# Optimization experiments

Hardware: AMD Instinct MI355X
Metric: run time of the kernel (lower is better)

## Reference

```python
import jax, jax.numpy as jnp
import numpy as np
import math

B, N, H = 2, 2048, 256
NUM_HEADS, HEAD_DIM = 8, 32
WIN = 32            # window_size
WIN_LEN = 2 * WIN + 1


def setup_inputs() -> dict:
    key = jax.random.key(0)
    ks = jax.random.split(key, 12)
    s = 0.02
    return {
        "x": jax.random.normal(ks[0], (B, N, 4, H), dtype=jnp.float32),
        "Wq": jax.random.normal(ks[1], (H, H), dtype=jnp.float32) * s,
        "bq": jnp.zeros((H,), jnp.float32),
        "Wk": jax.random.normal(ks[2], (H, H), dtype=jnp.float32) * s,
        "bk": jnp.zeros((H,), jnp.float32),
        "Wv": jax.random.normal(ks[3], (H, H), dtype=jnp.float32) * s,
        "bv": jnp.zeros((H,), jnp.float32),
        "Wo": jax.random.normal(ks[4], (H, 3 * H), dtype=jnp.float32) * s,
        "bo": jnp.zeros((3 * H,), jnp.float32),
        "Wvec": jax.random.normal(ks[5], (H, 2 * H), dtype=jnp.float32) * s,
        "alpha_dot": jnp.float32(1.0),
        "alpha_norm": jnp.float32(1.0),
        "Wg": jax.random.normal(ks[6], (2 * H, H), dtype=jnp.float32) * s,
        "bg": jnp.zeros((H,), jnp.float32),
    }


def reference(x, Wq, bq, Wk, bk, Wv, bv, Wo, bo, Wvec, alpha_dot, alpha_norm, Wg, bg):
    h, d = NUM_HEADS, HEAD_DIM
    scale = 1.0 / math.sqrt(d)

    x_scalar = x[:, :, 0]          # (B,N,H)
    vec = x[:, :, 1:4]             # (B,N,3,H)

    q = (x_scalar @ Wq + bq).reshape(B, N, h, d).transpose(0, 2, 1, 3)  # (B,h,N,d)
    k = (x_scalar @ Wk + bk).reshape(B, N, h, d).transpose(0, 2, 1, 3)
    v = (x_scalar @ Wv + bv).reshape(B, N, h, d).transpose(0, 2, 1, 3)

    vec_proj = vec @ Wvec                                # (B,N,3,2H)
    vec1, vec2 = vec_proj[..., :H], vec_proj[..., H:]
    vec_dot = (vec1 * vec2).sum(axis=-2)                 # (B,N,H)
    vec_norm = jnp.linalg.norm(vec, axis=2)              # (B,N,H)

    # (B,N,3,h,d) -> (B,h,N,3*d)
    vec_flat = vec.reshape(B, N, 3, h, d).transpose(0, 3, 1, 2, 4).reshape(B, h, N, 3 * d)

    # sliding-window attention via padded gather (matches torch unfold semantics)
    BH = B * h
    q_l = q.reshape(BH, N, d)
    k_l = k.reshape(BH, N, d)
    v_l = v.reshape(BH, N, d)
    vec_l = vec_flat.reshape(BH, N, 3 * d)

    pad = ((0, 0), (WIN, WIN), (0, 0))
    k_p = jnp.pad(k_l, pad)
    v_p = jnp.pad(v_l, pad)
    vec_p = jnp.pad(vec_l, pad)

    idx = jnp.arange(N)[:, None] + jnp.arange(WIN_LEN)[None, :]  # (N,WIN_LEN)
    k_win = k_p[:, idx]        # (BH,N,WIN_LEN,d)
    v_win = v_p[:, idx]
    vec_win = vec_p[:, idx]    # (BH,N,WIN_LEN,3d)

    attn_scores = jnp.einsum('bid,biwd->biw', q_l, k_win) * scale
    attn_weights = jax.nn.softmax(attn_scores, axis=-1)  # (BH,N,WIN_LEN)

    x_agg = jnp.einsum('biw,biwd->bid', attn_weights, v_win).reshape(B, h, N, d)
    vec_aggr = jnp.einsum('biw,biwd->bid', attn_weights, vec_win).reshape(B, h, N, 3 * d)

    x_out = x_agg.transpose(0, 2, 1, 3).reshape(B, N, H)
    vec_aggr = vec_aggr.reshape(B, h, N, 3, d).transpose(0, 2, 3, 1, 4).reshape(B, N, 3, H)

    invariants = jnp.concatenate([alpha_dot * vec_dot, alpha_norm * vec_norm], axis=-1)
    gate = jax.nn.sigmoid(invariants @ Wg + bg)[:, :, None, :]   # (B,N,1,H)
    vec_combined = gate * vec_aggr + vec                          # gated add mixing

    o = x_out @ Wo + bo
    o1, o2, o3 = o[..., :H], o[..., H:2 * H], o[..., 2 * H:]
    x_updated = vec_dot * o1 + vec_norm * o2 + o3

    x_final = jnp.concatenate([x_updated[:, :, None], vec_combined], axis=2)  # (B,N,4,H)
    return x_final, attn_weights
```

## Files before the change

kernel.cpp:

```cpp
#include <hip/hip_runtime.h>
#include <hip/hip_bf16.h>
#include <math.h>

#define Bc 2
#define Nn 2048
#define Hh 256
#define NH 8
#define Dd 32
#define WIN 32
#define WL 65
#define BN (Bc * Nn)

typedef __attribute__((ext_vector_type(8))) short bf16x8;
typedef __attribute__((ext_vector_type(4))) float f32x4;

__device__ inline short f2bf(float f) {
    union { float f; unsigned u; } v; v.f = f;
    unsigned r = v.u + 0x7fffu + ((v.u >> 16) & 1u);
    return (short)(r >> 16);
}

__device__ inline bf16x8 cvt8(float4 a, float4 b) {
    union { __hip_bfloat162 h[4]; bf16x8 v; } u;
    u.h[0] = __float22bfloat162_rn(make_float2(a.x, a.y));
    u.h[1] = __float22bfloat162_rn(make_float2(a.z, a.w));
    u.h[2] = __float22bfloat162_rn(make_float2(b.x, b.y));
    u.h[3] = __float22bfloat162_rn(make_float2(b.z, b.w));
    return u.v;
}

__global__ __launch_bounds__(256) void castw_kernel(
    const float* __restrict__ Wq, const float* __restrict__ Wk, const float* __restrict__ Wv,
    const float* __restrict__ Wvec, const float* __restrict__ Wg, const float* __restrict__ Wo,
    short* __restrict__ WqkvT, short* __restrict__ WvecT,
    short* __restrict__ WgT, short* __restrict__ WoT) {
    __shared__ float Ts[32][33];
    const int t = threadIdx.x;
    const int cc = t & 31, r0 = t >> 5;
    const int id = blockIdx.x;
    const float* W; int ldw; short* WT; int ldwt; int n0s, k0, n0d;
    if (id < 192) {
        const int tn = id >> 3, tk = id & 7, sel = tn >> 3;
        W = sel == 0 ? Wq : (sel == 1 ? Wk : Wv); ldw = 256;
        n0s = (tn & 7) * 32; k0 = tk * 32; WT = WqkvT; ldwt = 256; n0d = tn * 32;
    } else if (id < 320) {
        const int id2 = id - 192, tn = id2 >> 3, tk = id2 & 7;
        W = Wvec; ldw = 512; n0s = tn * 32; k0 = tk * 32; WT = WvecT; ldwt = 256; n0d = n0s;
    } else if (id < 448) {
        const int id3 = id - 320, tn = id3 >> 4, tk = id3 & 15;
        W = Wg; ldw = 256; n0s = tn * 32; k0 = tk * 32; WT = WgT; ldwt = 512; n0d = n0s;
    } else {
        const int id4 = id - 448, tn = id4 >> 3, tk = id4 & 7;
        W = Wo; ldw = 768; n0s = tn * 32; k0 = tk * 32; WT = WoT; ldwt = 256; n0d = n0s;
    }
#pragma unroll
    for (int p = 0; p < 4; ++p) {
        const int rr = r0 + p * 8;
        Ts[rr][cc] = W[(size_t)(k0 + rr) * ldw + n0s + cc];
    }
    __syncthreads();
#pragma unroll
    for (int p = 0; p < 4; ++p) {
        const int rr = r0 + p * 8;
        WT[(size_t)(n0d + rr) * ldwt + k0 + cc] = f2bf(Ts[cc][rr]);
    }
}

__global__ __launch_bounds__(256) void fused_mid(
    const float* __restrict__ x,
    const short* __restrict__ WqkvT, const short* __restrict__ WvecT,
    const short* __restrict__ WgT,
    const float* __restrict__ bq, const float* __restrict__ bk, const float* __restrict__ bv,
    const float* __restrict__ alpha_dot, const float* __restrict__ alpha_norm,
    const float* __restrict__ bg,
    short* __restrict__ Qb, short* __restrict__ Kb, short* __restrict__ Vb,
    float* __restrict__ vec_dot, float* __restrict__ vec_norm, float* __restrict__ gate) {
    __shared__ __align__(16) short lds[31232];
    const int bid = blockIdx.x;
    const int t = threadIdx.x, lane = t & 63, wid = t >> 6;
    const int quad = lane >> 4, lm = lane & 15;

    if (bid < 384) {
        short* As = lds;
        short* Bs = lds + 2560;
        const int rb = bid & 63, cb = bid >> 6;
        const int row0 = rb * 64, col0 = cb * 128;
        const int wm = wid & 1, wn = wid >> 1;
        const int srow = t >> 2, scg = (t & 3) * 8;
        f32x4 acc[2][4];
#pragma unroll
        for (int mt = 0; mt < 2; ++mt)
#pragma unroll
            for (int nt = 0; nt < 4; ++nt) {
                f32x4 z = {0.f, 0.f, 0.f, 0.f};
                acc[mt][nt] = z;
            }
        float4 pa0 = *(const float4*)&x[(size_t)(row0 + srow) * 1024 + scg];
        float4 pa1 = *(const float4*)&x[(size_t)(row0 + srow) * 1024 + scg + 4];
        bf16x8 pb[2];
#pragma unroll
        for (int p = 0; p < 2; ++p) {
            const int idx = t + p * 256;
            pb[p] = *(const bf16x8*)&WqkvT[(size_t)(col0 + (idx >> 2)) * 256 + (idx & 3) * 8];
        }
        for (int k0 = 0; k0 < 256; k0 += 32) {
            *(bf16x8*)&As[srow * 40 + scg] = cvt8(pa0, pa1);
#pragma unroll
            for (int p = 0; p < 2; ++p) {
                const int idx = t + p * 256;
                *(bf16x8*)&Bs[(idx >> 2) * 40 + (idx & 3) * 8] = pb[p];
            }
            __syncthreads();
            if (k0 + 32 < 256) {
                pa0 = *(const float4*)&x[(size_t)(row0 + srow) * 1024 + k0 + 32 + scg];
                pa1 = *(const float4*)&x[(size_t)(row0 + srow) * 1024 + k0 + 32 + scg + 4];
#pragma unroll
                for (int p = 0; p < 2; ++p) {
                    const int idx = t + p * 256;
                    pb[p] = *(const bf16x8*)&WqkvT[(size_t)(col0 + (idx >> 2)) * 256 + k0 + 32 + (idx & 3) * 8];
                }
            }
            bf16x8 af[2], bfr[4];
#pragma unroll
            for (int mt = 0; mt < 2; ++mt)
                af[mt] = *(bf16x8*)&As[(wm * 32 + mt * 16 + lm) * 40 + quad * 8];
#pragma unroll
            for (int nt = 0; nt < 4; ++nt)
                bfr[nt] = *(bf16x8*)&Bs[(wn * 64 + nt * 16 + lm) * 40 + quad * 8];
#pragma unroll
            for (int mt = 0; mt < 2; ++mt)
#pragma unroll
                for (int nt = 0; nt < 4; ++nt)
                    acc[mt][nt] = __builtin_amdgcn_mfma_f32_16x16x32_bf16(
                        af[mt], bfr[nt], acc[mt][nt], 0, 0, 0);
            __syncthreads();
        }
        const int chunk = col0 >> 8;
        short* dst = chunk == 0 ? Qb : (chunk == 1 ? Kb : Vb);
        const float* bias = chunk == 0 ? bq : (chunk == 1 ? bk : bv);
#pragma unroll
        for (int mt = 0; mt < 2; ++mt)
#pragma unroll
            for (int nt = 0; nt < 4; ++nt) {
                const int col = col0 + (wid >> 1) * 64 + nt * 16 + lm;
                const int cm = col & 255;
                const float bb = bias[cm];
#pragma unroll
                for (int r = 0; r < 4; ++r) {
                    const int row = row0 + (wid & 1) * 32 + mt * 16 + quad * 4 + r;
                    dst[(size_t)row * 256 + cm] = f2bf(acc[mt][nt][r] + bb);
                }
            }
        return;
    }

    short* As    = lds;
    short* Bs    = lds + 12672;
    short* inv_s = lds + 22912;
    const int row0 = (bid - 384) * 16;

#pragma unroll
    for (int it = 0; it < 6; ++it) {
        const int idx = t + it * 256;
        const int p = idx >> 9, rem = idx & 511, row = rem >> 5, kg = rem & 31;
        const float* src = &x[(size_t)(row0 + row) * 1024 + (1 + p) * 256 + kg * 8];
        *(bf16x8*)&As[(p * 16 + row) * 264 + kg * 8] =
            cvt8(*(const float4*)src, *(const float4*)(src + 4));
    }
    const float an = alpha_norm[0], ad = alpha_dot[0];
#pragma unroll
    for (int it = 0; it < 4; ++it) {
        const int idx = t + it * 256;
        const int row = idx >> 6, c4 = idx & 63;
        const size_t xb = (size_t)(row0 + row) * 1024 + c4 * 4;
        const float4 v0 = *(const float4*)&x[xb + 256];
        const float4 v1 = *(const float4*)&x[xb + 512];
        const float4 v2 = *(const float4*)&x[xb + 768];
        float4 nr;
        nr.x = sqrtf(v0.x * v0.x + v1.x * v1.x + v2.x * v2.x);
        nr.y = sqrtf(v0.y * v0.y + v1.y * v1.y + v2.y * v2.y);
        nr.z = sqrtf(v0.z * v0.z + v1.z * v1.z + v2.z * v2.z);
        nr.w = sqrtf(v0.w * v0.w + v1.w * v1.w + v2.w * v2.w);
        *(float4*)&vec_norm[(size_t)(row0 + row) * 256 + c4 * 4] = nr;
        short* ip = &inv_s[row * 520 + 256 + c4 * 4];
        ip[0] = f2bf(an * nr.x); ip[1] = f2bf(an * nr.y);
        ip[2] = f2bf(an * nr.z); ip[3] = f2bf(an * nr.w);
    }
    __syncthreads();

    for (int cg = 0; cg < 2; ++cg) {
        f32x4 acc[3][2][2];
#pragma unroll
        for (int p = 0; p < 3; ++p)
#pragma unroll
            for (int h = 0; h < 2; ++h)
#pragma unroll
                for (int nt = 0; nt < 2; ++nt) {
                    f32x4 z = {0.f, 0.f, 0.f, 0.f};
                    acc[p][h][nt] = z;
                }
        bf16x8 pb[4];
#pragma unroll
        for (int q = 0; q < 4; ++q) {
            const int idx = t + q * 256;
            const int h = idx >> 9, rem = idx & 511, col = rem >> 2, kg = rem & 3;
            pb[q] = *(const bf16x8*)&WvecT[(size_t)(h * 256 + cg * 128 + col) * 256 + kg * 8];
        }
        for (int k0 = 0; k0 < 256; k0 += 32) {
#pragma unroll
            for (int q = 0; q < 4; ++q) {
                const int idx = t + q * 256;
                const int h = idx >> 9, rem = idx & 511, col = rem >> 2, kg = rem & 3;
                *(bf16x8*)&Bs[(h * 128 + col) * 40 + kg * 8] = pb[q];
            }
            __syncthreads();
            if (k0 + 32 < 256) {
#pragma unroll
                for (int q = 0; q < 4; ++q) {
                    const int idx = t + q * 256;
                    const int h = idx >> 9, rem = idx & 511, col = rem >> 2, kg = rem & 3;
                    pb[q] = *(const bf16x8*)&WvecT[(size_t)(h * 256 + cg * 128 + col) * 256 + k0 + 32 + kg * 8];
                }
            }
            bf16x8 af[3], bfr[2][2];
#pragma unroll
            for (int p = 0; p < 3; ++p)
                af[p] = *(bf16x8*)&As[(p * 16 + lm) * 264 + k0 + quad * 8];
#pragma unroll
            for (int h = 0; h < 2; ++h)
#pragma unroll
                for (int nt = 0; nt < 2; ++nt)
                    bfr[h][nt] = *(bf16x8*)&Bs[(h * 128 + wid * 32 + nt * 16 + lm) * 40 + quad * 8];
#pragma unroll
            for (int p = 0; p < 3; ++p)
#pragma unroll
                for (int h = 0; h < 2; ++h)
#pragma unroll
                    for (int nt = 0; nt < 2; ++nt)
                        acc[p][h][nt] = __builtin_amdgcn_mfma_f32_16x16x32_bf16(
                            af[p], bfr[h][nt], acc[p][h][nt], 0, 0, 0);
            __syncthreads();
        }
#pragma unroll
        for (int nt = 0; nt < 2; ++nt) {
            const int col = cg * 128 + wid * 32 + nt * 16 + lm;
#pragma unroll
            for (int r = 0; r < 4; ++r) {
                const int row = quad * 4 + r;
                float dot = 0.f;
#pragma unroll
                for (int p = 0; p < 3; ++p)
                    dot = fmaf(acc[p][0][nt][r], acc[p][1][nt][r], dot);
                vec_dot[(size_t)(row0 + row) * 256 + col] = dot;
                inv_s[row * 520 + col] = f2bf(ad * dot);
            }
        }
        __syncthreads();
    }

    f32x4 g[4];
#pragma unroll
    for (int nt = 0; nt < 4; ++nt) {
        f32x4 z = {0.f, 0.f, 0.f, 0.f};
        g[nt] = z;
    }
    bf16x8 pg[4];
#pragma unroll
    for (int q = 0; q < 4; ++q) {
        const int idx = t + q * 256;
        pg[q] = *(const bf16x8*)&WgT[(size_t)(idx >> 2) * 512 + (idx & 3) * 8];
    }
    for (int k0 = 0; k0 < 512; k0 += 32) {
#pragma unroll
        for (int q = 0; q < 4; ++q) {
            const int idx = t + q * 256;
            *(bf16x8*)&Bs[(idx >> 2) * 40 + (idx & 3) * 8] = pg[q];
        }
        __syncthreads();
        if (k0 + 32 < 512) {
#pragma unroll
            for (int q = 0; q < 4; ++q) {
                const int idx = t + q * 256;
                pg[q] = *(const bf16x8*)&WgT[(size_t)(idx >> 2) * 512 + k0 + 32 + (idx & 3) * 8];
            }
        }
        const bf16x8 ai = *(bf16x8*)&inv_s[lm * 520 + k0 + quad * 8];
#pragma unroll
        for (int nt = 0; nt < 4; ++nt) {
            const bf16x8 bgf = *(bf16x8*)&Bs[(wid * 64 + nt * 16 + lm) * 40 + quad * 8];
            g[nt] = __builtin_amdgcn_mfma_f32_16x16x32_bf16(ai, bgf, g[nt], 0, 0, 0);
        }
        __syncthreads();
    }
#pragma unroll
    for (int nt = 0; nt < 4; ++nt) {
        const int col = wid * 64 + nt * 16 + lm;
        const float bb = bg[col];
#pragma unroll
        for (int r = 0; r < 4; ++r) {
            const int row = row0 + quad * 4 + r;
            const float z = g[nt][r] + bb;
            gate[(size_t)row * 256 + col] = 1.f / (1.f + __expf(-z));
        }
    }
}

__global__ __launch_bounds__(256) void attn_fused(
    const short* __restrict__ Qb, const short* __restrict__ Kb,
    const short* __restrict__ Vb,
    const float* __restrict__ gate, const float* __restrict__ x,
    float* __restrict__ attnw, float* __restrict__ out, short* __restrict__ xout_bf) {
    const int bh = blockIdx.x >> 6, tile = blockIdx.x & 63;
    const int b = bh >> 3, hd = bh & 7;
    const int i0 = tile * 32;
    const int t = threadIdx.x, lane = t & 63, wid = t >> 6;
    const int wm = wid & 1, wn = wid >> 1, quad = lane >> 4, lm = lane & 15;

    __shared__ __align__(16) short Qs[32 * 40];
    __shared__ __align__(16) short Ks[96 * 40];
    __shared__ __align__(16) short Pb[32 * 104];
    __shared__ __align__(16) short St[128 * 104];

    for (int idx = t; idx < 32 * 104 / 2; idx += 256) ((int*)Pb)[idx] = 0;
    if (t < 128) {
        const int row = t >> 2, cg = t & 3;
        *(bf16x8*)&Qs[row * 40 + cg * 8] =
            *(const bf16x8*)&Qb[((size_t)(b * Nn + i0 + row)) * 256 + hd * 32 + cg * 8];
    }
#pragma unroll
    for (int kk = 0; kk < 2; ++kk) {
        const int idx = t + kk * 256;
        if (idx < 384) {
            const int row = idx >> 2, cg = idx & 3;
            const int j = i0 - WIN + row;
            bf16x8 kv = {0, 0, 0, 0, 0, 0, 0, 0};
            if (j >= 0 && j < Nn)
                kv = *(const bf16x8*)&Kb[((size_t)(b * Nn + j)) * 256 + hd * 32 + cg * 8];
            *(bf16x8*)&Ks[row * 40 + cg * 8] = kv;
        }
    }
    __syncthreads();

    if (wid < 2) {
        const int il0 = wid * 16;
        const bf16x8 aq = *(bf16x8*)&Qs[(il0 + lm) * 40 + quad * 8];
        f32x4 c[6];
#pragma unroll
        for (int nt = 0; nt < 6; ++nt) {
            const bf16x8 bk = *(bf16x8*)&Ks[(nt * 16 + lm) * 40 + quad * 8];
            f32x4 z = {0.f, 0.f, 0.f, 0.f};
            c[nt] = __builtin_amdgcn_mfma_f32_16x16x32_bf16(aq, bk, z, 0, 0, 0);
        }
        float mx[4] = {-1e30f, -1e30f, -1e30f, -1e30f};
#pragma unroll
        for (int nt = 0; nt < 6; ++nt)
#pragma unroll
            for (int r = 0; r < 4; ++r) {
                const int il = il0 + quad * 4 + r;
                const int w = nt * 16 + lm - il;
                const float v = (w >= 0 && w <= 64)
                    ? c[nt][r] * 0.17677669529663687f : -1e30f;
                c[nt][r] = v;
                mx[r] = fmaxf(mx[r], v);
            }
#pragma unroll
        for (int off = 1; off < 16; off <<= 1)
#pragma unroll
            for (int r = 0; r < 4; ++r) mx[r] = fmaxf(mx[r], __shfl_xor(mx[r], off, 64));
        float sm[4] = {0.f, 0.f, 0.f, 0.f};
#pragma unroll
        for (int nt = 0; nt < 6; ++nt)
#pragma unroll
            for (int r = 0; r < 4; ++r) {
                const int il = il0 + quad * 4 + r;
                const int w = nt * 16 + lm - il;
                const float e = (w >= 0 && w <= 64) ? __expf(c[nt][r] - mx[r]) : 0.f;
                c[nt][r] = e;
                sm[r] += e;
            }
#pragma unroll
        for (int off = 1; off < 16; off <<= 1)
#pragma unroll
            for (int r = 0; r < 4; ++r) sm[r] += __shfl_xor(sm[r], off, 64);
        float inv[4];
#pragma unroll
        for (int r = 0; r < 4; ++r) inv[r] = 1.f / sm[r];
#pragma unroll
        for (int nt = 0; nt < 6; ++nt)
#pragma unroll
            for (int r = 0; r < 4; ++r) {
                const int il = il0 + quad * 4 + r;
                const int jr = nt * 16 + lm;
                const int w = jr - il;
                if (w >= 0 && w <= 64) {
                    const float pw = c[nt][r] * inv[r];
                    attnw[((size_t)bh * Nn + (i0 + il)) * WL + w] = pw;
                    Pb[il * 104 + jr] = f2bf(pw);
                }
            }
    } else {
        const int tt = t - 128;
        const int chunk = tt >> 3, j0 = tt & 7;
#pragma unroll
        for (int it = 0; it < 12; ++it) {
            const int jr = j0 + it * 8;
            const int j = i0 - WIN + jr;
            bf16x8 val = {0, 0, 0, 0, 0, 0, 0, 0};
            if (j >= 0 && j < Nn) {
                if (chunk < 4) {
                    val = *(const bf16x8*)&Vb[((size_t)(b * Nn + j)) * 256 + hd * 32 + chunk * 8];
                } else {
                    const int vc = (chunk - 4) >> 2, d0 = ((chunk - 4) & 3) * 8;
                    const float* src = &x[((size_t)(b * Nn + j)) * 1024 + (1 + vc) * 256 + hd * 32 + d0];
                    val = cvt8(*(const float4*)src, *(const float4*)(src + 4));
                }
            }
#pragma unroll
            for (int u = 0; u < 8; ++u) St[(chunk * 8 + u) * 104 + jr] = val[u];
        }
    }
    __syncthreads();

    f32x4 acc[4];
#pragma unroll
    for (int nt = 0; nt < 4; ++nt) {
        f32x4 z = {0.f, 0.f, 0.f, 0.f};
        acc[nt] = z;
    }
#pragma unroll
    for (int ks = 0; ks < 3; ++ks) {
        const bf16x8 ap = *(bf16x8*)&Pb[(wm * 16 + lm) * 104 + ks * 32 + quad * 8];
#pragma unroll
        for (int nt = 0; nt < 4; ++nt) {
            const bf16x8 bs = *(bf16x8*)&St[(wn * 64 + nt * 16 + lm) * 104 + ks * 32 + quad * 8];
            acc[nt] = __builtin_amdgcn_mfma_f32_16x16x32_bf16(ap, bs, acc[nt], 0, 0, 0);
        }
    }
#pragma unroll
    for (int nt = 0; nt < 4; ++nt) {
        const int dim = wn * 64 + nt * 16 + lm;
#pragma unroll
        for (int r = 0; r < 4; ++r) {
            const int i = wm * 16 + quad * 4 + r;
            const size_t bn = (size_t)(b * Nn + i0 + i);
            if (dim < 32) {
                xout_bf[bn * 256 + hd * 32 + dim] = f2bf(acc[nt][r]);
            } else {
                const int dm = dim - 32, c = dm >> 5, dd = dm & 31;
                const int ch = hd * 32 + dd;
                const float g = gate[bn * 256 + ch];
                const size_t off = bn * 1024 + (1 + c) * 256 + ch;
                out[off] = fmaf(g, acc[nt][r], x[off]);
            }
        }
    }
}

__global__ __launch_bounds__(256) void gemm_outf(
    const short* __restrict__ A, const short* __restrict__ BT,
    const float* __restrict__ bo,
    const float* __restrict__ vec_dot, const float* __restrict__ vec_norm,
    float* __restrict__ out) {
    __shared__ short As[64 * 40];
    __shared__ short Bs[3][64 * 40];
    const int row0 = blockIdx.x * 64, ch0 = blockIdx.y * 64;
    const int t = threadIdx.x, lane = t & 63, wid = t >> 6;
    const int wm = wid & 1, wn = wid >> 1, quad = lane >> 4, lm = lane & 15;
    const int srow = t >> 2, scg = (t & 3) * 8;
    f32x4 acc[3][2][2];
#pragma unroll
    for (int p = 0; p < 3; ++p)
#pragma unroll
        for (int mt = 0; mt < 2; ++mt)
#pragma unroll
            for (int nt = 0; nt < 2; ++nt) {
                f32x4 z = {0.f, 0.f, 0.f, 0.f};
                acc[p][mt][nt] = z;
            }
    bf16x8 pa, pb[3];
    pa = *(const bf16x8*)&A[(size_t)(row0 + srow) * 256 + scg];
#pragma unroll
    for (int p = 0; p < 3; ++p)
        pb[p] = *(const bf16x8*)&BT[(size_t)(p * 256 + ch0 + srow) * 256 + scg];
    for (int k0 = 0; k0 < 256; k0 += 32) {
        *(bf16x8*)&As[srow * 40 + scg] = pa;
#pragma unroll
        for (int p = 0; p < 3; ++p)
            *(bf16x8*)&Bs[p][srow * 40 + scg] = pb[p];
        __syncthreads();
        if (k0 + 32 < 256) {
            pa = *(const bf16x8*)&A[(size_t)(row0 + srow) * 256 + k0 + 32 + scg];
#pragma unroll
            for (int p = 0; p < 3; ++p)
                pb[p] = *(const bf16x8*)&BT[(size_t)(p * 256 + ch0 + srow) * 256 + k0 + 32 + scg];
        }
        bf16x8 af[2], bfr[3][2];
#pragma unroll
        for (int mt = 0; mt < 2; ++mt)
            af[mt] = *(bf16x8*)&As[(wm * 32 + mt * 16 + lm) * 40 + quad * 8];
#pragma unroll
        for (int p = 0; p < 3; ++p)
#pragma unroll
            for (int nt = 0; nt < 2; ++nt)
                bfr[p][nt] = *(bf16x8*)&Bs[p][(wn * 32 + nt * 16 + lm) * 40 + quad * 8];
#pragma unroll
        for (int p = 0; p < 3; ++p)
#pragma unroll
            for (int mt = 0; mt < 2; ++mt)
#pragma unroll
                for (int nt = 0; nt < 2; ++nt)
                    acc[p][mt][nt] = __builtin_amdgcn_mfma_f32_16x16x32_bf16(
                        af[mt], bfr[p][nt], acc[p][mt][nt], 0, 0, 0);
        __syncthreads();
    }
#pragma unroll
    for (int mt = 0; mt < 2; ++mt)
#pragma unroll
        for (int nt = 0; nt < 2; ++nt) {
            const int col = ch0 + wn * 32 + nt * 16 + lm;
            const float b1 = bo[col], b2 = bo[256 + col], b3 = bo[512 + col];
#pragma unroll
            for (int r = 0; r < 4; ++r) {
                const int row = row0 + wm * 32 + mt * 16 + quad * 4 + r;
                const float o1 = acc[0][mt][nt][r] + b1;
                const float o2 = acc[1][mt][nt][r] + b2;
                const float o3 = acc[2][mt][nt][r] + b3;
                const float vd = vec_dot[(size_t)row * 256 + col];
                const float vn = vec_norm[(size_t)row * 256 + col];
                out[(size_t)row * 1024 + col] = vd * o1 + vn * o2 + o3;
            }
        }
}

extern "C" void kernel_launch(void* const* d_in, const int* in_sizes, int n_in,
                              void* d_out, int out_size, void* d_ws, size_t ws_size,
                              hipStream_t stream) {
    const float* x  = (const float*)d_in[0];
    const float* Wq = (const float*)d_in[1];
    const float* bq = (const float*)d_in[2];
    const float* Wk = (const float*)d_in[3];
    const float* bk = (const float*)d_in[4];
    const float* Wv = (const float*)d_in[5];
    const float* bv = (const float*)d_in[6];
    const float* Wo = (const float*)d_in[7];
    const float* bo = (const float*)d_in[8];
    const float* Wvec = (const float*)d_in[9];
    const float* alpha_dot  = (const float*)d_in[10];
    const float* alpha_norm = (const float*)d_in[11];
    const float* Wg = (const float*)d_in[12];
    const float* bg = (const float*)d_in[13];

    float* ws = (float*)d_ws;
    float* vec_dot  = ws;
    float* vec_norm = ws + 1048576;
    float* gate     = ws + 2097152;
    short* sb = (short*)(ws + 3145728);
    short* xout_bf = sb;
    short* Q_bf    = sb + 1048576;
    short* K_bf    = sb + 2097152;
    short* V_bf    = sb + 3145728;
    short* WqkvT   = sb + 4194304;
    short* WvecT   = sb + 4390912;
    short* WgT     = sb + 4521984;
    short* WoT     = sb + 4653056;

    float* out = (float*)d_out;
    float* attnw = out + (size_t)Bc * Nn * 4 * Hh;

    castw_kernel<<<640, 256, 0, stream>>>(Wq, Wk, Wv, Wvec, Wg, Wo,
                                          WqkvT, WvecT, WgT, WoT);
    fused_mid<<<640, 256, 0, stream>>>(x, WqkvT, WvecT, WgT, bq, bk, bv,
                                       alpha_dot, alpha_norm, bg,
                                       Q_bf, K_bf, V_bf, vec_dot, vec_norm, gate);
    attn_fused<<<1024, 256, 0, stream>>>(Q_bf, K_bf, V_bf, gate, x,
                                         attnw, out, xout_bf);
    gemm_outf<<<dim3(64, 4), 256, 0, stream>>>(xout_bf, WoT, bo, vec_dot, vec_norm, out);
}
```

Before: 154.8 us.

## Redistribute vec-norm, vec-dot, gate GEMM across kernels for better parallelism

Moves the vector-norm computation into the weight-cast prep kernel and retiles the vec_dot GEMM in the middle kernel into 64x32 output tiles, giving 512 blocks instead of 256 blocks of 16 rows. The gate GEMM now runs as its own block range alongside attention in a combined kernel. Attention writes vec_aggr to a workspace buffer, and the gated residual add moves into the output GEMM kernel. This is meant to raise occupancy and parallelism in the mid stage, at the cost of extra global round trips for inv_bf and vec_aggr (about 12 MB more traffic).

```diff
diff --git a/kernel.cpp b/kernel.cpp
--- a/kernel.cpp
+++ b/kernel.cpp
@@ -12,6 +12,7 @@
 #define BN (Bc * Nn)
 
 typedef __attribute__((ext_vector_type(8))) short bf16x8;
+typedef __attribute__((ext_vector_type(4))) short s16x4;
 typedef __attribute__((ext_vector_type(4))) float f32x4;
 
 __device__ inline short f2bf(float f) {
@@ -29,13 +30,35 @@
     return u.v;
 }
 
-__global__ __launch_bounds__(256) void castw_kernel(
+__global__ __launch_bounds__(256) void prep_kernel(
+    const float* __restrict__ x, const float* __restrict__ alpha_norm,
     const float* __restrict__ Wq, const float* __restrict__ Wk, const float* __restrict__ Wv,
     const float* __restrict__ Wvec, const float* __restrict__ Wg, const float* __restrict__ Wo,
+    float* __restrict__ vec_norm, short* __restrict__ inv_bf,
     short* __restrict__ WqkvT, short* __restrict__ WvecT,
     short* __restrict__ WgT, short* __restrict__ WoT) {
     __shared__ float Ts[32][33];
     const int t = threadIdx.x;
+    if (blockIdx.x >= 640) {
+        const int gid = (blockIdx.x - 640) * 256 + t;
+        const int bn = gid >> 6, c4 = gid & 63;
+        const size_t base = (size_t)bn * 1024 + c4 * 4;
+        const float4 v0 = *(const float4*)&x[base + 256];
+        const float4 v1 = *(const float4*)&x[base + 512];
+        const float4 v2 = *(const float4*)&x[base + 768];
+        float4 nr;
+        nr.x = sqrtf(v0.x * v0.x + v1.x * v1.x + v2.x * v2.x);
+        nr.y = sqrtf(v0.y * v0.y + v1.y * v1.y + v2.y * v2.y);
+        nr.z = sqrtf(v0.z * v0.z + v1.z * v1.z + v2.z * v2.z);
+        nr.w = sqrtf(v0.w * v0.w + v1.w * v1.w + v2.w * v2.w);
+        *(float4*)&vec_norm[(size_t)bn * 256 + c4 * 4] = nr;
+        const float an = alpha_norm[0];
+        s16x4 iv;
+        iv[0] = f2bf(an * nr.x); iv[1] = f2bf(an * nr.y);
+        iv[2] = f2bf(an * nr.z); iv[3] = f2bf(an * nr.w);
+        *(s16x4*)&inv_bf[(size_t)bn * 512 + 256 + c4 * 4] = iv;
+        return;
+    }
     const int cc = t & 31, r0 = t >> 5;
     const int id = blockIdx.x;
     const float* W; int ldw; short* WT; int ldwt; int n0s, k0, n0d;
@@ -66,27 +89,23 @@
     }
 }
 
-__global__ __launch_bounds__(256) void fused_mid(
+__global__ __launch_bounds__(256) void mid_kernel(
     const float* __restrict__ x,
     const short* __restrict__ WqkvT, const short* __restrict__ WvecT,
-    const short* __restrict__ WgT,
     const float* __restrict__ bq, const float* __restrict__ bk, const float* __restrict__ bv,
-    const float* __restrict__ alpha_dot, const float* __restrict__ alpha_norm,
-    const float* __restrict__ bg,
+    const float* __restrict__ alpha_dot,
     short* __restrict__ Qb, short* __restrict__ Kb, short* __restrict__ Vb,
-    float* __restrict__ vec_dot, float* __restrict__ vec_norm, float* __restrict__ gate) {
-    __shared__ __align__(16) short lds[31232];
+    float* __restrict__ vec_dot, short* __restrict__ inv_bf) {
+    __shared__ __align__(16) short lds[10240];
     const int bid = blockIdx.x;
     const int t = threadIdx.x, lane = t & 63, wid = t >> 6;
-    const int quad = lane >> 4, lm = lane & 15;
+    const int wm = wid & 1, wn = wid >> 1, quad = lane >> 4, lm = lane & 15;
+    const int srow = t >> 2, scg = (t & 3) * 8;
 
     if (bid < 384) {
         short* As = lds;
         short* Bs = lds + 2560;
-        const int rb = bid & 63, cb = bid >> 6;
-        const int row0 = rb * 64, col0 = cb * 128;
-        const int wm = wid & 1, wn = wid >> 1;
-        const int srow = t >> 2, scg = (t & 3) * 8;
+        const int row0 = (bid & 63) * 64, col0 = (bid >> 6) * 128;
         f32x4 acc[2][4];
 #pragma unroll
         for (int mt = 0; mt < 2; ++mt)
@@ -142,184 +161,163 @@
         for (int mt = 0; mt < 2; ++mt)
 #pragma unroll
             for (int nt = 0; nt < 4; ++nt) {
-                const int col = col0 + (wid >> 1) * 64 + nt * 16 + lm;
-                const int cm = col & 255;
+                const int cm = (col0 + wn * 64 + nt * 16 + lm) & 255;
                 const float bb = bias[cm];
 #pragma unroll
                 for (int r = 0; r < 4; ++r) {
-                    const int row = row0 + (wid & 1) * 32 + mt * 16 + quad * 4 + r;
+                    const int row = row0 + wm * 32 + mt * 16 + quad * 4 + r;
                     dst[(size_t)row * 256 + cm] = f2bf(acc[mt][nt][r] + bb);
                 }
             }
         return;
     }
 
-    short* As    = lds;
-    short* Bs    = lds + 12672;
-    short* inv_s = lds + 22912;
-    const int row0 = (bid - 384) * 16;
-
-#pragma unroll
-    for (int it = 0; it < 6; ++it) {
-        const int idx = t + it * 256;
-        const int p = idx >> 9, rem = idx & 511, row = rem >> 5, kg = rem & 31;
-        const float* src = &x[(size_t)(row0 + row) * 1024 + (1 + p) * 256 + kg * 8];
-        *(bf16x8*)&As[(p * 16 + row) * 264 + kg * 8] =
-            cvt8(*(const float4*)src, *(const float4*)(src + 4));
-    }
-    const float an = alpha_norm[0], ad = alpha_dot[0];
-#pragma unroll
-    for (int it = 0; it < 4; ++it) {
-        const int idx = t + it * 256;
-        const int row = idx >> 6, c4 = idx & 63;
-        const size_t xb = (size_t)(row0 + row) * 1024 + c4 * 4;
-        const float4 v0 = *(const float4*)&x[xb + 256];
-        const float4 v1 = *(const float4*)&x[xb + 512];
-        const float4 v2 = *(const float4*)&x[xb + 768];
-        float4 nr;
-        nr.x = sqrtf(v0.x * v0.x + v1.x * v1.x + v2.x * v2.x);
-        nr.y = sqrtf(v0.y * v0.y + v1.y * v1.y + v2.y * v2.y);
-        nr.z = sqrtf(v0.z * v0.z + v1.z * v1.z + v2.z * v2.z);
-        nr.w = sqrtf(v0.w * v0.w + v1.w * v1.w + v2.w * v2.w);
-        *(float4*)&vec_norm[(size_t)(row0 + row) * 256 + c4 * 4] = nr;
-        short* ip = &inv_s[row * 520 + 256 + c4 * 4];
-        ip[0] = f2bf(an * nr.x); ip[1] = f2bf(an * nr.y);
-        ip[2] = f2bf(an * nr.z); ip[3] = f2bf(an * nr.w);
-    }
-    __syncthreads();
-
-    for (int cg = 0; cg < 2; ++cg) {
-        f32x4 acc[3][2][2];
+    short* As = lds;
+    short* Bs = lds + 7680;
+    const int vb = bid - 384;
+    const int row0 = (vb >> 3) * 64, ch0 = (vb & 7) * 32;
+    const int bh_ = t >> 7, bc = (t >> 2) & 31, bcg = (t & 3) * 8;
+    f32x4 acc[3][2][2];
+#pragma unroll
+    for (int p = 0; p < 3; ++p)
+#pragma unroll
+        for (int h = 0; h < 2; ++h)
+#pragma unroll
+            for (int mt = 0; mt < 2; ++mt) {
+                f32x4 z = {0.f, 0.f, 0.f, 0.f};
+                acc[p][h][mt] = z;
+            }
+    float4 pa0[3], pa1[3];
+#pragma unroll
+    for (int p = 0; p < 3; ++p) {
+        pa0[p] = *(const float4*)&x[(size_t)(row0 + srow) * 1024 + (1 + p) * 256 + scg];
+        pa1[p] = *(const float4*)&x[(size_t)(row0 + srow) * 1024 + (1 + p) * 256 + scg + 4];
+    }
+    bf16x8 pb = *(const bf16x8*)&WvecT[(size_t)(bh_ * 256 + ch0 + bc) * 256 + bcg];
+    for (int k0 = 0; k0 < 256; k0 += 32) {
 #pragma unroll
         for (int p = 0; p < 3; ++p)
+            *(bf16x8*)&As[p * 2560 + srow * 40 + scg] = cvt8(pa0[p], pa1[p]);
+        *(bf16x8*)&Bs[bh_ * 1280 + bc * 40 + bcg] = pb;
+        __syncthreads();
+        if (k0 + 32 < 256) {
+#pragma unroll
+            for (int p = 0; p < 3; ++p) {
+                pa0[p] = *(const float4*)&x[(size_t)(row0 + srow) * 1024 + (1 + p) * 256 + k0 + 32 + scg];
+                pa1[p] = *(const float4*)&x[(size_t)(row0 + srow) * 1024 + (1 + p) * 256 + k0 + 32 + scg + 4];
+            }
+            pb = *(const bf16x8*)&WvecT[(size_t)(bh_ * 256 + ch0 + bc) * 256 + k0 + 32 + bcg];
+        }
+        bf16x8 af[3][2], bfr[2];
+#pragma unroll
+        for (int p = 0; p < 3; ++p)
+#pragma unroll
+            for (int mt = 0; mt < 2; ++mt)
+                af[p][mt] = *(bf16x8*)&As[p * 2560 + (wm * 32 + mt * 16 + lm) * 40 + quad * 8];
+#pragma unroll
+        for (int h = 0; h < 2; ++h)
+            bfr[h] = *(bf16x8*)&Bs[h * 1280 + (wn * 16 + lm) * 40 + quad * 8];
+#pragma unroll
+        for (int p = 0; p < 3; ++p)
 #pragma unroll
             for (int h = 0; h < 2; ++h)
 #pragma unroll
-                for (int nt = 0; nt < 2; ++nt) {
-                    f32x4 z = {0.f, 0.f, 0.f, 0.f};
-                    acc[p][h][nt] = z;
+                for (int mt = 0; mt < 2; ++mt)
+                    acc[p][h][mt] = __builtin_amdgcn_mfma_f32_16x16x32_bf16(
+                        af[p][mt], bfr[h], acc[p][h][mt], 0, 0, 0);
+        __syncthreads();
+    }
+    const float ad = alpha_dot[0];
+#pragma unroll
+    for (int mt = 0; mt < 2; ++mt) {
+        const int col = ch0 + wn * 16 + lm;
+#pragma unroll
+        for (int r = 0; r < 4; ++r) {
+            const int row = row0 + wm * 32 + mt * 16 + quad * 4 + r;
+            float dot = 0.f;
+#pragma unroll
+            for (int p = 0; p < 3; ++p)
+                dot = fmaf(acc[p][0][mt][r], acc[p][1][mt][r], dot);
+            vec_dot[(size_t)row * 256 + col] = dot;
+            inv_bf[(size_t)row * 512 + col] = f2bf(ad * dot);
+        }
+    }
+}
+
+__global__ __launch_bounds__(256) void gate_attn_kernel(
+    const short* __restrict__ inv_bf, const short* __restrict__ WgT,
+    const float* __restrict__ bg,
+    const short* __restrict__ Qb, const short* __restrict__ Kb,
+    const short* __restrict__ Vb, const float* __restrict__ x,
+    float* __restrict__ gate, float* __restrict__ attnw,
+    float* __restrict__ vec_aggr, short* __restrict__ xout_bf) {
+    __shared__ __align__(16) short lds[21760];
+    const int bid = blockIdx.x;
+    const int t = threadIdx.x, lane = t & 63, wid = t >> 6;
+    const int wm = wid & 1, wn = wid >> 1, quad = lane >> 4, lm = lane & 15;
+
+    if (bid < 256) {
+        short* As = lds;
+        short* Bs = lds + 2560;
+        const int row0 = (bid & 63) * 64, col0 = (bid >> 6) * 64;
+        const int srow = t >> 2, scg = (t & 3) * 8;
+        f32x4 acc[2][2];
+#pragma unroll
+        for (int mt = 0; mt < 2; ++mt)
+#pragma unroll
+            for (int nt = 0; nt < 2; ++nt) {
+                f32x4 z = {0.f, 0.f, 0.f, 0.f};
+                acc[mt][nt] = z;
+            }
+        bf16x8 pa = *(const bf16x8*)&inv_bf[(size_t)(row0 + srow) * 512 + scg];
+        bf16x8 pb = *(const bf16x8*)&WgT[(size_t)(col0 + srow) * 512 + scg];
+        for (int k0 = 0; k0 < 512; k0 += 32) {
+            *(bf16x8*)&As[srow * 40 + scg] = pa;
+            *(bf16x8*)&Bs[srow * 40 + scg] = pb;
+            __syncthreads();
+            if (k0 + 32 < 512) {
+                pa = *(const bf16x8*)&inv_bf[(size_t)(row0 + srow) * 512 + k0 + 32 + scg];
+                pb = *(const bf16x8*)&WgT[(size_t)(col0 + srow) * 512 + k0 + 32 + scg];
+            }
+            bf16x8 af[2], bfr[2];
+#pragma unroll
+            for (int mt = 0; mt < 2; ++mt)
+                af[mt] = *(bf16x8*)&As[(wm * 32 + mt * 16 + lm) * 40 + quad * 8];
+#pragma unroll
+            for (int nt = 0; nt < 2; ++nt)
+                bfr[nt] = *(bf16x8*)&Bs[(wn * 32 + nt * 16 + lm) * 40 + quad * 8];
+#pragma unroll
+            for (int mt = 0; mt < 2; ++mt)
+#pragma unroll
+                for (int nt = 0; nt < 2; ++nt)
+                    acc[mt][nt] = __builtin_amdgcn_mfma_f32_16x16x32_bf16(
+                        af[mt], bfr[nt], acc[mt][nt], 0, 0, 0);
+            __syncthreads();
+        }
+#pragma unroll
+        for (int mt = 0; mt < 2; ++mt)
+#pragma unroll
+            for (int nt = 0; nt < 2; ++nt) {
+                const int col = col0 + wn * 32 + nt * 16 + lm;
+                const float bb = bg[col];
+#pragma unroll
+                for (int r = 0; r < 4; ++r) {
+                    const int row = row0 + wm * 32 + mt * 16 + quad * 4 + r;
+                    const float z = acc[mt][nt][r] + bb;
+                    gate[(size_t)row * 256 + col] = 1.f / (1.f + __expf(-z));
                 }
-        bf16x8 pb[4];
-#pragma unroll
-        for (int q = 0; q < 4; ++q) {
-            const int idx = t + q * 256;
-            const int h = idx >> 9, rem = idx & 511, col = rem >> 2, kg = rem & 3;
-            pb[q] = *(const bf16x8*)&WvecT[(size_t)(h * 256 + cg * 128 + col) * 256 + kg * 8];
-        }
-        for (int k0 = 0; k0 < 256; k0 += 32) {
-#pragma unroll
-            for (int q = 0; q < 4; ++q) {
-                const int idx = t + q * 256;
-                const int h = idx >> 9, rem = idx & 511, col = rem >> 2, kg = rem & 3;
-                *(bf16x8*)&Bs[(h * 128 + col) * 40 + kg * 8] = pb[q];
-            }
-            __syncthreads();
-            if (k0 + 32 < 256) {
-#pragma unroll
-                for (int q = 0; q < 4; ++q) {
-                    const int idx = t + q * 256;
-                    const int h = idx >> 9, rem = idx & 511, col = rem >> 2, kg = rem & 3;
-                    pb[q] = *(const bf16x8*)&WvecT[(size_t)(h * 256 + cg * 128 + col) * 256 + k0 + 32 + kg * 8];
-                }
-            }
-            bf16x8 af[3], bfr[2][2];
-#pragma unroll
-            for (int p = 0; p < 3; ++p)
-                af[p] = *(bf16x8*)&As[(p * 16 + lm) * 264 + k0 + quad * 8];
-#pragma unroll
-            for (int h = 0; h < 2; ++h)
-#pragma unroll
-                for (int nt = 0; nt < 2; ++nt)
-                    bfr[h][nt] = *(bf16x8*)&Bs[(h * 128 + wid * 32 + nt * 16 + lm) * 40 + quad * 8];
-#pragma unroll
-            for (int p = 0; p < 3; ++p)
-#pragma unroll
-                for (int h = 0; h < 2; ++h)
-#pragma unroll
-                    for (int nt = 0; nt < 2; ++nt)
-                        acc[p][h][nt] = __builtin_amdgcn_mfma_f32_16x16x32_bf16(
-                            af[p], bfr[h][nt], acc[p][h][nt], 0, 0, 0);
-            __syncthreads();
-        }
-#pragma unroll
-        for (int nt = 0; nt < 2; ++nt) {
-            const int col = cg * 128 + wid * 32 + nt * 16 + lm;
-#pragma unroll
-            for (int r = 0; r < 4; ++r) {
-                const int row = quad * 4 + r;
-                float dot = 0.f;
-#pragma unroll
-                for (int p = 0; p < 3; ++p)
-                    dot = fmaf(acc[p][0][nt][r], acc[p][1][nt][r], dot);
-                vec_dot[(size_t)(row0 + row) * 256 + col] = dot;
-                inv_s[row * 520 + col] = f2bf(ad * dot);
-            }
-        }
-        __syncthreads();
-    }
-
-    f32x4 g[4];
-#pragma unroll
-    for (int nt = 0; nt < 4; ++nt) {
-        f32x4 z = {0.f, 0.f, 0.f, 0.f};
-        g[nt] = z;
-    }
-    bf16x8 pg[4];
-#pragma unroll
-    for (int q = 0; q < 4; ++q) {
-        const int idx = t + q * 256;
-        pg[q] = *(const bf16x8*)&WgT[(size_t)(idx >> 2) * 512 + (idx & 3) * 8];
-    }
-    for (int k0 = 0; k0 < 512; k0 += 32) {
-#pragma unroll
-        for (int q = 0; q < 4; ++q) {
-            const int idx = t + q * 256;
-            *(bf16x8*)&Bs[(idx >> 2) * 40 + (idx & 3) * 8] = pg[q];
-        }
-        __syncthreads();
-        if (k0 + 32 < 512) {
-#pragma unroll
-            for (int q = 0; q < 4; ++q) {
-                const int idx = t + q * 256;
-                pg[q] = *(const bf16x8*)&WgT[(size_t)(idx >> 2) * 512 + k0 + 32 + (idx & 3) * 8];
-            }
-        }
-        const bf16x8 ai = *(bf16x8*)&inv_s[lm * 520 + k0 + quad * 8];
-#pragma unroll
-        for (int nt = 0; nt < 4; ++nt) {
-            const bf16x8 bgf = *(bf16x8*)&Bs[(wid * 64 + nt * 16 + lm) * 40 + quad * 8];
-            g[nt] = __builtin_amdgcn_mfma_f32_16x16x32_bf16(ai, bgf, g[nt], 0, 0, 0);
-        }
-        __syncthreads();
-    }
-#pragma unroll
-    for (int nt = 0; nt < 4; ++nt) {
-        const int col = wid * 64 + nt * 16 + lm;
-        const float bb = bg[col];
-#pragma unroll
-        for (int r = 0; r < 4; ++r) {
-            const int row = row0 + quad * 4 + r;
-            const float z = g[nt][r] + bb;
-            gate[(size_t)row * 256 + col] = 1.f / (1.f + __expf(-z));
-        }
-    }
-}
-
-__global__ __launch_bounds__(256) void attn_fused(
-    const short* __restrict__ Qb, const short* __restrict__ Kb,
-    const short* __restrict__ Vb,
-    const float* __restrict__ gate, const float* __restrict__ x,
-    float* __restrict__ attnw, float* __restrict__ out, short* __restrict__ xout_bf) {
-    const int bh = blockIdx.x >> 6, tile = blockIdx.x & 63;
+            }
+        return;
+    }
+
+    short* Qs = lds;
+    short* Ks = lds + 1280;
+    short* Pb = lds + 5120;
+    short* St = lds + 8448;
+    const int ab = bid - 256;
+    const int bh = ab >> 6, tile = ab & 63;
     const int b = bh >> 3, hd = bh & 7;
     const int i0 = tile * 32;
-    const int t = threadIdx.x, lane = t & 63, wid = t >> 6;
-    const int wm = wid & 1, wn = wid >> 1, quad = lane >> 4, lm = lane & 15;
-
-    __shared__ __align__(16) short Qs[32 * 40];
-    __shared__ __align__(16) short Ks[96 * 40];
-    __shared__ __align__(16) short Pb[32 * 104];
-    __shared__ __align__(16) short St[128 * 104];
 
     for (int idx = t; idx < 32 * 104 / 2; idx += 256) ((int*)Pb)[idx] = 0;
     if (t < 128) {
@@ -447,23 +445,21 @@
                 xout_bf[bn * 256 + hd * 32 + dim] = f2bf(acc[nt][r]);
             } else {
                 const int dm = dim - 32, c = dm >> 5, dd = dm & 31;
-                const int ch = hd * 32 + dd;
-                const float g = gate[bn * 256 + ch];
-                const size_t off = bn * 1024 + (1 + c) * 256 + ch;
-                out[off] = fmaf(g, acc[nt][r], x[off]);
-            }
-        }
-    }
-}
-
-__global__ __launch_bounds__(256) void gemm_outf(
+                vec_aggr[((size_t)c * BN + bn) * 256 + hd * 32 + dd] = acc[nt][r];
+            }
+        }
+    }
+}
+
+__global__ __launch_bounds__(256) void out_kernel(
     const short* __restrict__ A, const short* __restrict__ BT,
     const float* __restrict__ bo,
     const float* __restrict__ vec_dot, const float* __restrict__ vec_norm,
-    float* __restrict__ out) {
+    const float* __restrict__ gate, const float* __restrict__ vec_aggr,
+    const float* __restrict__ x, float* __restrict__ out) {
     __shared__ short As[64 * 40];
     __shared__ short Bs[3][64 * 40];
-    const int row0 = blockIdx.x * 64, ch0 = blockIdx.y * 64;
+    const int row0 = (blockIdx.x & 63) * 64, ch0 = (blockIdx.x >> 6) * 64;
     const int t = threadIdx.x, lane = t & 63, wid = t >> 6;
     const int wm = wid & 1, wn = wid >> 1, quad = lane >> 4, lm = lane & 15;
     const int srow = t >> 2, scg = (t & 3) * 8;
@@ -530,6 +526,23 @@
                 out[(size_t)row * 1024 + col] = vd * o1 + vn * o2 + o3;
             }
         }
+#pragma unroll
+    for (int c = 0; c < 3; ++c) {
+#pragma unroll
+        for (int it = 0; it < 4; ++it) {
+            const int idx = t + it * 256;
+            const int row = row0 + (idx >> 4), col = ch0 + (idx & 15) * 4;
+            const float4 g4 = *(const float4*)&gate[(size_t)row * 256 + col];
+            const float4 va = *(const float4*)&vec_aggr[((size_t)c * BN + row) * 256 + col];
+            const float4 xv = *(const float4*)&x[(size_t)row * 1024 + (1 + c) * 256 + col];
+            float4 o;
+            o.x = fmaf(g4.x, va.x, xv.x);
+            o.y = fmaf(g4.y, va.y, xv.y);
+            o.z = fmaf(g4.z, va.z, xv.z);
+            o.w = fmaf(g4.w, va.w, xv.w);
+            *(float4*)&out[(size_t)row * 1024 + (1 + c) * 256 + col] = o;
+        }
+    }
 }
 
 extern "C" void kernel_launch(void* const* d_in, const int* in_sizes, int n_in,
@@ -554,25 +567,27 @@
     float* vec_dot  = ws;
     float* vec_norm = ws + 1048576;
     float* gate     = ws + 2097152;
-    short* sb = (short*)(ws + 3145728);
+    float* vec_aggr = ws + 3145728;
+    short* sb = (short*)(ws + 6291456);
     short* xout_bf = sb;
     short* Q_bf    = sb + 1048576;
     short* K_bf    = sb + 2097152;
     short* V_bf    = sb + 3145728;
-    short* WqkvT   = sb + 4194304;
-    short* WvecT   = sb + 4390912;
-    short* WgT     = sb + 4521984;
-    short* WoT     = sb + 4653056;
+    short* inv_bf  = sb + 4194304;
+    short* WqkvT   = sb + 6291456;
+    short* WvecT   = sb + 6488064;
+    short* WgT     = sb + 6619136;
+    short* WoT     = sb + 6750208;
 
     float* out = (float*)d_out;
     float* attnw = out + (size_t)Bc * Nn * 4 * Hh;
 
-    castw_kernel<<<640, 256, 0, stream>>>(Wq, Wk, Wv, Wvec, Wg, Wo,
-                                          WqkvT, WvecT, WgT, WoT);
-    fused_mid<<<640, 256, 0, stream>>>(x, WqkvT, WvecT, WgT, bq, bk, bv,
-                                       alpha_dot, alpha_norm, bg,
-                                       Q_bf, K_bf, V_bf, vec_dot, vec_norm, gate);
-    attn_fused<<<1024, 256, 0, stream>>>(Q_bf, K_bf, V_bf, gate, x,
-                                         attnw, out, xout_bf);
-    gemm_outf<<<dim3(64, 4), 256, 0, stream>>>(xout_bf, WoT, bo, vec_dot, vec_norm, out);
-}
+    prep_kernel<<<1664, 256, 0, stream>>>(x, alpha_norm, Wq, Wk, Wv, Wvec, Wg, Wo,
+                                          vec_norm, inv_bf, WqkvT, WvecT, WgT, WoT);
+    mid_kernel<<<896, 256, 0, stream>>>(x, WqkvT, WvecT, bq, bk, bv, alpha_dot,
+                                        Q_bf, K_bf, V_bf, vec_dot, inv_bf);
+    gate_attn_kernel<<<1280, 256, 0, stream>>>(inv_bf, WgT, bg, Q_bf, K_bf, V_bf, x,
+                                               gate, attnw, vec_aggr, xout_bf);
+    out_kernel<<<256, 256, 0, stream>>>(xout_bf, WoT, bo, vec_dot, vec_norm,
+                                        gate, vec_aggr, x, out);
+}
```

Result: no change. 157.4 us (+1.7%).
